# Kernel tuning notes

Hardware: AMD Instinct MI355X
Metric: run time of the kernel (lower is better)

Reference implementation:

```python
import jax, jax.numpy as jnp
import numpy as np

N_NODES = 50000
N_EDGES = 156000
D_IN = 512
D_OUT = 512
NUM_RELATIONS = 3
EPS = 0.0  # GIN eps, train_eps=False


def setup_inputs() -> dict:
    key = jax.random.key(0)
    ks = jax.random.split(key, 10)
    s = 1.0 / np.sqrt(D_IN)
    so = 1.0 / np.sqrt(D_OUT)
    return {
        "x": jax.random.normal(ks[0], (N_NODES, D_IN), dtype=jnp.float32),
        "edge_index": jax.random.randint(ks[1], (2, N_EDGES), 0, N_NODES, dtype=jnp.int64),
        "edge_type": jax.random.randint(ks[2], (N_EDGES,), 0, NUM_RELATIONS, dtype=jnp.int64),
        # self-loop linear
        "W_self": jax.random.uniform(ks[3], (D_IN, D_OUT), jnp.float32, -s, s),
        "b_self": jax.random.uniform(ks[4], (D_OUT,), jnp.float32, -s, s),
        # per-relation GIN MLP: Linear(D_IN,D_OUT) -> ReLU -> Linear(D_OUT,D_OUT)
        "W1": jax.random.uniform(ks[5], (NUM_RELATIONS, D_IN, D_OUT), jnp.float32, -s, s),
        "b1": jax.random.uniform(ks[6], (NUM_RELATIONS, D_OUT), jnp.float32, -s, s),
        "W2": jax.random.uniform(ks[7], (NUM_RELATIONS, D_OUT, D_OUT), jnp.float32, -so, so),
        "b2": jax.random.uniform(ks[8], (NUM_RELATIONS, D_OUT), jnp.float32, -so, so),
    }


def reference(x, edge_index, edge_type, W_self, b_self, W1, b1, W2, b2):
    n_nodes = x.shape[0]
    src, dst = edge_index[0], edge_index[1]
    x_src = x[src]  # [E, D_IN] single gather shared across relations
    out = x @ W_self + b_self  # self-loop linear, [N, D_OUT]
    for r in range(NUM_RELATIONS):
        mask = (edge_type == r).astype(x.dtype)[:, None]  # [E,1]
        # GIN sum-aggregation restricted to relation r edges
        agg = jax.ops.segment_sum(x_src * mask, dst, num_segments=n_nodes)  # [N, D_IN]
        h = (1.0 + EPS) * x + agg
        h = jnp.maximum(h @ W1[r] + b1[r], 0.0) @ W2[r] + b2[r]  # MLP
        out = out + h
    return out
```

## Files before the change

### kernel.cpp

```cpp
#include <hip/hip_runtime.h>
#include <hip/hip_bf16.h>

typedef __attribute__((ext_vector_type(8))) short bfrag_t;
typedef __attribute__((ext_vector_type(4))) float accum_t;
typedef __attribute__((ext_vector_type(8))) unsigned short us8_t;

static_assert(sizeof(bfrag_t) == 16, "frag size");

static constexpr int M_NODES = 50000;
static constexpr int E_EDGES = 156000;
static constexpr int MT256   = 196;
static constexpr int M_PAD   = MT256 * 256;

__device__ __forceinline__ unsigned short f2bf(float f) {
  unsigned int u = __float_as_uint(f);
  u = (u + 0x7FFFu + ((u >> 16) & 1u)) >> 16;
  return (unsigned short)u;
}
__device__ __forceinline__ float bf2f(unsigned short u) {
  return __uint_as_float(((unsigned int)u) << 16);
}

__device__ __forceinline__ void gll16(const unsigned short* g, unsigned short* l) {
  __builtin_amdgcn_global_load_lds(
      (const __attribute__((address_space(1))) void*)g,
      (__attribute__((address_space(3))) void*)l,
      16, 0, 0);
}

typedef __attribute__((ext_vector_type(2))) short s2v;
__device__ __forceinline__ void agg_atomic_add(unsigned int* p, unsigned int zv) {
#if __has_builtin(__builtin_amdgcn_global_atomic_fadd_v2bf16)
  s2v v;
  __builtin_memcpy(&v, &zv, 4);
  __builtin_amdgcn_global_atomic_fadd_v2bf16(
      (__attribute__((address_space(1))) s2v*)p, v);
#else
  unsigned int old = *p, assumed;
  do {
    assumed = old;
    float lo = bf2f((unsigned short)(assumed & 0xffffu)) +
               bf2f((unsigned short)(zv & 0xffffu));
    float hi = bf2f((unsigned short)(assumed >> 16)) +
               bf2f((unsigned short)(zv >> 16));
    unsigned int nv = (unsigned int)f2bf(lo) | ((unsigned int)f2bf(hi) << 16);
    old = atomicCAS(p, assumed, nv);
  } while (old != assumed);
#endif
}

__global__ void cast_w_kernel(const float* __restrict__ Wself,
                              const float* __restrict__ W1,
                              const float* __restrict__ W2,
                              const float* __restrict__ b2,
                              unsigned short* __restrict__ Wt1k,
                              unsigned short* __restrict__ Wt2k,
                              float* __restrict__ bias2) {
  int idx = blockIdx.x * 256 + threadIdx.x;
  if (idx < 1048576) {
    int j   = idx & 7;
    int n   = (idx >> 3) & 2047;
    int kcg = idx >> 14;
    int k   = kcg * 8 + j;
    float v = (n < 512)
        ? Wself[k * 512 + n]
        : W1[(size_t)((n - 512) >> 9) * 262144 + k * 512 + ((n - 512) & 511)];
    Wt1k[idx] = f2bf(v);
  } else if (idx < 1835008) {
    int j2  = idx - 1048576;
    int j   = j2 & 7;
    int n   = (j2 >> 3) & 511;
    int kcg = j2 >> 12;
    int kk  = kcg * 8 + j;
    Wt2k[j2] = f2bf(W2[(size_t)(kk >> 9) * 262144 + (size_t)(kk & 511) * 512 + n]);
  } else if (idx < 1835520) {
    int c = idx - 1835008;
    bias2[c] = b2[c] + b2[512 + c] + b2[1024 + c];
  }
}

__global__ __launch_bounds__(256) void cast_xk_kernel(const float* __restrict__ x,
                                                      unsigned short* __restrict__ xk) {
  __shared__ unsigned short T[32][520];
  const int b   = blockIdx.x;
  const int tid = threadIdx.x;
  for (int j = 0; j < 16; ++j) {
    int idx = j * 256 + tid;
    int row = idx >> 7, c4 = idx & 127;
    int grow = b * 32 + row;
    float4 v = (grow < M_NODES) ? ((const float4*)(x + (size_t)grow * 512))[c4]
                                : make_float4(0.f, 0.f, 0.f, 0.f);
    unsigned short* t = &T[row][c4 * 4];
    t[0] = f2bf(v.x); t[1] = f2bf(v.y); t[2] = f2bf(v.z); t[3] = f2bf(v.w);
  }
  __syncthreads();
  for (int j = 0; j < 8; ++j) {
    int idx = j * 256 + tid;
    int kc = idx >> 5, row = idx & 31;
    *(us8_t*)&xk[((size_t)kc * M_PAD + b * 32 + row) * 8] = *(const us8_t*)&T[row][kc * 8];
  }
}

__global__ void scatter_all_kernel(const unsigned short* __restrict__ Z,
                                   const int* __restrict__ ei,
                                   const int* __restrict__ et,
                                   unsigned short* __restrict__ agg) {
  int e    = blockIdx.x * 4 + (threadIdx.x >> 6);
  int lane = threadIdx.x & 63;
  if (e >= E_EDGES) return;
  int rel = et[e];
  int src = ei[e];
  int dst = ei[E_EDGES + e];
  const unsigned int* zs = (const unsigned int*)(Z + (size_t)src * 1536 + rel * 512);
  unsigned int* ad = (unsigned int*)(agg + (size_t)dst * 1536 + rel * 512);
  unsigned int v[4];
#pragma unroll
  for (int j = 0; j < 4; ++j) v[j] = zs[j * 64 + lane];
#pragma unroll
  for (int j = 0; j < 4; ++j) agg_atomic_add(ad + j * 64 + lane, v[j]);
}

__global__ void relu_all_kernel(unsigned short* __restrict__ Z,
                                const unsigned short* __restrict__ agg,
                                const float* __restrict__ b1) {
  int i = blockIdx.x * 256 + threadIdx.x;
  if (i >= M_NODES * 192) return;
  int c = (i % 192) * 8;
  us8_t z = ((const us8_t*)Z)[i];
  us8_t a = ((const us8_t*)agg)[i];
  us8_t o;
#pragma unroll
  for (int j = 0; j < 8; ++j) {
    float v = bf2f((unsigned short)z[j]) + bf2f((unsigned short)a[j]) + b1[c + j];
    o[j] = f2bf(fmaxf(v, 0.f));
  }
  ((us8_t*)Z)[i] = o;
}

__global__ __launch_bounds__(512, 4) void gemm1_kernel(
    const unsigned short* __restrict__ Ak,
    const unsigned short* __restrict__ Bk,
    float* __restrict__ outF,
    unsigned short* __restrict__ outB,
    const float* __restrict__ biasF) {
  constexpr int NT = 16, NTC = 16;
  __shared__ alignas(16) unsigned short L[3][12288];
  const int tid  = threadIdx.x;
  const int lane = tid & 63;
  const int wid  = tid >> 6;
  const int wr   = wid >> 1;
  const int wn   = wid & 1;
  const int fr   = lane & 15;
  const int kcl  = lane >> 4;

  constexpr int nwg = MT256 * NTC;
  constexpr int q   = nwg / 8;
  const int orig = blockIdx.x;
  const int swz  = (orig & 7) * q + (orig >> 3);
  const int tileM = (swz / NTC) * 256;
  const int tileN = (swz % NTC) * 128;

  accum_t acc[4][4] = {};

  const unsigned short* gA = Ak + ((size_t)(tid >> 8) * M_PAD + tileM + (tid & 255)) * 8;
  const unsigned short* gB = Bk + ((size_t)(tid >> 7) * 2048 + tileN + (tid & 127)) * 8;
  constexpr size_t AKT = (size_t)4 * M_PAD * 8;
  constexpr size_t A2  = (size_t)2 * M_PAD * 8;
  constexpr size_t BKT = (size_t)4 * 2048 * 8;

#define STG(buf, kt) do {                                            \
    gll16(gA + (size_t)(kt) * AKT,      &L[buf][tid * 8]);           \
    gll16(gA + (size_t)(kt) * AKT + A2, &L[buf][tid * 8 + 4096]);    \
    gll16(gB + (size_t)(kt) * BKT,      &L[buf][8192 + tid * 8]);    \
  } while (0)

  const int aoff = kcl * 2048 + (wr * 64 + fr) * 8;
  const int boff = 8192 + kcl * 1024 + (wn * 64 + fr) * 8;

  STG(0, 0); STG(1, 1);

  for (int kt = 0; kt < NT; ++kt) {
    if (kt + 1 < NT) asm volatile("s_waitcnt vmcnt(3)" ::: "memory");
    else             asm volatile("s_waitcnt vmcnt(0)" ::: "memory");
    __builtin_amdgcn_s_barrier();

    const unsigned short* Ls = &L[kt % 3][0];
    bfrag_t b[4], a[4];
#pragma unroll
    for (int nf = 0; nf < 4; ++nf)
      b[nf] = *(const bfrag_t*)(Ls + boff + nf * 128);
#pragma unroll
    for (int mf = 0; mf < 4; ++mf)
      a[mf] = *(const bfrag_t*)(Ls + aoff + mf * 128);
    if (kt + 2 < NT) STG((kt + 2) % 3, kt + 2);
    __builtin_amdgcn_s_setprio(1);
#pragma unroll
    for (int mf = 0; mf < 4; ++mf)
#pragma unroll
      for (int nf = 0; nf < 4; ++nf)
        acc[mf][nf] = __builtin_amdgcn_mfma_f32_16x16x32_bf16(a[mf], b[nf], acc[mf][nf], 0, 0, 0);
    __builtin_amdgcn_s_setprio(0);
  }
#undef STG

  __syncthreads();

  const int rq = lane >> 4;
  if (tileN >= 512) {
    unsigned short* Wld = &L[0][0] + wid * 4608;
#pragma unroll
    for (int mf = 0; mf < 4; ++mf)
#pragma unroll
      for (int nf = 0; nf < 4; ++nf)
#pragma unroll
        for (int p = 0; p < 4; ++p)
          Wld[(mf * 16 + rq * 4 + p) * 72 + nf * 16 + fr] = f2bf(acc[mf][nf][p]);
    const int r8 = lane >> 3;
    const int ch = lane & 7;
    const size_t zc = (size_t)(tileN - 512) + wn * 64 + ch * 8;
#pragma unroll
    for (int pass = 0; pass < 8; ++pass) {
      const int lrow = pass * 8 + r8;
      const int grow = tileM + wr * 64 + lrow;
      us8_t v = *(const us8_t*)&Wld[lrow * 72 + ch * 8];
      if (grow < M_NODES)
        *(us8_t*)&outB[(size_t)grow * 1536 + zc] = v;
    }
  } else {
#pragma unroll
    for (int nf = 0; nf < 4; ++nf) {
      const int col = tileN + wn * 64 + nf * 16 + fr;
      const float bv = biasF[col];
#pragma unroll
      for (int mf = 0; mf < 4; ++mf) {
        const int rbase = tileM + wr * 64 + mf * 16 + rq * 4;
#pragma unroll
        for (int p = 0; p < 4; ++p) {
          const int row = rbase + p;
          if (row < M_NODES)
            outF[(size_t)row * 512 + col] = acc[mf][nf][p] + bv;
        }
      }
    }
  }
}

__global__ __launch_bounds__(512, 4) void gemm2_kernel(
    const unsigned short* __restrict__ A,
    const unsigned short* __restrict__ Bk,
    float* __restrict__ outF,
    const float* __restrict__ bias) {
  constexpr int KTOT = 1536, NT = 48, NTC = 4;
  __shared__ alignas(16) unsigned short L[3][12288];
  const int tid  = threadIdx.x;
  const int lane = tid & 63;
  const int wid  = tid >> 6;
  const int wr   = wid >> 1;
  const int wn   = wid & 1;
  const int fr   = lane & 15;
  const int kcl  = lane >> 4;

  constexpr int nwg = MT256 * NTC;
  constexpr int q   = nwg / 8;
  const int orig = blockIdx.x;
  const int swz  = (orig & 7) * q + (orig >> 3);
  const int tileM = (swz / NTC) * 256;
  const int tileN = (swz % NTC) * 128;

  accum_t acc[4][4] = {};

  const int rowS = tid & 255;
  int arow = tileM + rowS; arow = arow < M_NODES ? arow : M_NODES - 1;
  const unsigned short* gA = A + (size_t)arow * KTOT + (tid >> 8) * 8;
  const unsigned short* gB = Bk + ((size_t)(tid >> 7) * 512 + tileN + (tid & 127)) * 8;
  constexpr size_t BKT = (size_t)4 * 512 * 8;

#define STG(buf, kt) do {                                          \
    gll16(gA + (kt) * 32,               &L[buf][tid * 8]);         \
    gll16(gA + (kt) * 32 + 16,          &L[buf][tid * 8 + 4096]);  \
    gll16(gB + (size_t)(kt) * BKT,      &L[buf][8192 + tid * 8]);  \
  } while (0)

  const int aoff = kcl * 2048 + (wr * 64 + fr) * 8;
  const int boff = 8192 + kcl * 1024 + (wn * 64 + fr) * 8;

  STG(0, 0); STG(1, 1);

  for (int kt = 0; kt < NT; ++kt) {
    if (kt + 1 < NT) asm volatile("s_waitcnt vmcnt(3)" ::: "memory");
    else             asm volatile("s_waitcnt vmcnt(0)" ::: "memory");
    __builtin_amdgcn_s_barrier();

    const unsigned short* Ls = &L[kt % 3][0];
    bfrag_t b[4], a[4];
#pragma unroll
    for (int nf = 0; nf < 4; ++nf)
      b[nf] = *(const bfrag_t*)(Ls + boff + nf * 128);
#pragma unroll
    for (int mf = 0; mf < 4; ++mf)
      a[mf] = *(const bfrag_t*)(Ls + aoff + mf * 128);
    if (kt + 2 < NT) STG((kt + 2) % 3, kt + 2);
    __builtin_amdgcn_s_setprio(1);
#pragma unroll
    for (int mf = 0; mf < 4; ++mf)
#pragma unroll
      for (int nf = 0; nf < 4; ++nf)
        acc[mf][nf] = __builtin_amdgcn_mfma_f32_16x16x32_bf16(a[mf], b[nf], acc[mf][nf], 0, 0, 0);
    __builtin_amdgcn_s_setprio(0);
  }
#undef STG

  const int rq = lane >> 4;
#pragma unroll
  for (int nf = 0; nf < 4; ++nf) {
    const int col = tileN + wn * 64 + nf * 16 + fr;
    const float bv = bias[col];
#pragma unroll
    for (int mf = 0; mf < 4; ++mf) {
      const int rbase = tileM + wr * 64 + mf * 16 + rq * 4;
#pragma unroll
      for (int p = 0; p < 4; ++p) {
        const int row = rbase + p;
        if (row < M_NODES)
          outF[(size_t)row * 512 + col] += acc[mf][nf][p] + bv;
      }
    }
  }
}

extern "C" void kernel_launch(void* const* d_in, const int* in_sizes, int n_in,
                              void* d_out, int out_size, void* d_ws, size_t ws_size,
                              hipStream_t stream) {
  const float* x     = (const float*)d_in[0];
  const int*   ei    = (const int*)d_in[1];
  const int*   et    = (const int*)d_in[2];
  const float* Wself = (const float*)d_in[3];
  const float* bself = (const float*)d_in[4];
  const float* W1    = (const float*)d_in[5];
  const float* b1    = (const float*)d_in[6];
  const float* W2    = (const float*)d_in[7];
  const float* b2    = (const float*)d_in[8];
  float* out = (float*)d_out;

  char* ws = (char*)d_ws;
  unsigned short* xk    = (unsigned short*)ws;
  unsigned short* agg   = (unsigned short*)ws;
  unsigned short* Z     = (unsigned short*)(ws + 153600000);
  unsigned short* Wt1k  = (unsigned short*)(ws + 307200000);
  unsigned short* Wt2k  = (unsigned short*)(ws + 309297152);
  float*          bias2 = (float*)(ws + 310870016);

  cast_w_kernel<<<7171, 256, 0, stream>>>(Wself, W1, W2, b2, Wt1k, Wt2k, bias2);
  cast_xk_kernel<<<M_PAD / 32, 256, 0, stream>>>(x, xk);

  gemm1_kernel<<<MT256 * 16, 512, 0, stream>>>(xk, Wt1k, out, Z, bself);

  hipMemsetAsync(agg, 0, (size_t)M_NODES * 1536 * sizeof(unsigned short), stream);
  scatter_all_kernel<<<E_EDGES / 4, 256, 0, stream>>>(Z, ei, et, agg);
  relu_all_kernel<<<(M_NODES * 192 + 255) / 256, 256, 0, stream>>>(Z, agg, b1);

  gemm2_kernel<<<MT256 * 4, 512, 0, stream>>>(Z, Wt2k, out, bias2);
}
```

Measured before the change: 671.9 us.

## Transpose relu output into k-chunked layout and seed agg by copying Z

The relu kernel now reads only the aggregate buffer and writes its output through shared memory in a k-chunked, M-padded layout, so gemm2 can stage A with the same contiguous loads it uses for B. The aggregate buffer is initialised with a device copy of Z instead of a memset, which folds the self term into agg and lets relu skip reading Z. gemm1 gains an extra output pointer, but it is passed Z twice, so it writes the same data to the same address. The copy moves more bytes than a memset did, and Zk aliases Z, so relu overwrites Z after scatter has finished reading it.

Result: faster. 599.2 us (-10.8%).

```diff
diff --git a/kernel.cpp b/kernel.cpp
--- a/kernel.cpp
+++ b/kernel.cpp
@@ -120,21 +120,38 @@
   for (int j = 0; j < 4; ++j) agg_atomic_add(ad + j * 64 + lane, v[j]);
 }
 
-__global__ void relu_all_kernel(unsigned short* __restrict__ Z,
-                                const unsigned short* __restrict__ agg,
-                                const float* __restrict__ b1) {
-  int i = blockIdx.x * 256 + threadIdx.x;
-  if (i >= M_NODES * 192) return;
-  int c = (i % 192) * 8;
-  us8_t z = ((const us8_t*)Z)[i];
-  us8_t a = ((const us8_t*)agg)[i];
-  us8_t o;
-#pragma unroll
-  for (int j = 0; j < 8; ++j) {
-    float v = bf2f((unsigned short)z[j]) + bf2f((unsigned short)a[j]) + b1[c + j];
-    o[j] = f2bf(fmaxf(v, 0.f));
-  }
-  ((us8_t*)Z)[i] = o;
+__global__ __launch_bounds__(256) void relu_t_kernel(
+    const unsigned short* __restrict__ agg,
+    const float* __restrict__ b1,
+    unsigned short* __restrict__ Zk) {
+  __shared__ unsigned short T[16][1544];
+  const int b   = blockIdx.x;
+  const int tid = threadIdx.x;
+#pragma unroll
+  for (int j = 0; j < 12; ++j) {
+    int idx = j * 256 + tid;
+    int row = idx / 192, cc = idx % 192;
+    int grow = b * 16 + row;
+    us8_t o;
+    if (grow < M_NODES) {
+      us8_t a = ((const us8_t*)agg)[(size_t)grow * 192 + cc];
+      const float* bb = b1 + cc * 8;
+#pragma unroll
+      for (int q = 0; q < 8; ++q)
+        o[q] = f2bf(fmaxf(bf2f((unsigned short)a[q]) + bb[q], 0.f));
+    } else {
+#pragma unroll
+      for (int q = 0; q < 8; ++q) o[q] = 0;
+    }
+    *(us8_t*)&T[row][cc * 8] = o;
+  }
+  __syncthreads();
+#pragma unroll
+  for (int j = 0; j < 12; ++j) {
+    int idx = j * 256 + tid;
+    int kc = idx >> 4, row = idx & 15;
+    *(us8_t*)&Zk[((size_t)kc * M_PAD + b * 16 + row) * 8] = *(const us8_t*)&T[row][kc * 8];
+  }
 }
 
 __global__ __launch_bounds__(512, 4) void gemm1_kernel(
@@ -142,6 +159,7 @@
     const unsigned short* __restrict__ Bk,
     float* __restrict__ outF,
     unsigned short* __restrict__ outB,
+    unsigned short* __restrict__ aggB,
     const float* __restrict__ biasF) {
   constexpr int NT = 16, NTC = 16;
   __shared__ alignas(16) unsigned short L[3][12288];
@@ -223,8 +241,10 @@
       const int lrow = pass * 8 + r8;
       const int grow = tileM + wr * 64 + lrow;
       us8_t v = *(const us8_t*)&Wld[lrow * 72 + ch * 8];
-      if (grow < M_NODES)
+      if (grow < M_NODES) {
         *(us8_t*)&outB[(size_t)grow * 1536 + zc] = v;
+        *(us8_t*)&aggB[(size_t)grow * 1536 + zc] = v;
+      }
     }
   } else {
 #pragma unroll
@@ -246,11 +266,11 @@
 }
 
 __global__ __launch_bounds__(512, 4) void gemm2_kernel(
-    const unsigned short* __restrict__ A,
+    const unsigned short* __restrict__ Ak,
     const unsigned short* __restrict__ Bk,
     float* __restrict__ outF,
     const float* __restrict__ bias) {
-  constexpr int KTOT = 1536, NT = 48, NTC = 4;
+  constexpr int NT = 48, NTC = 4;
   __shared__ alignas(16) unsigned short L[3][12288];
   const int tid  = threadIdx.x;
   const int lane = tid & 63;
@@ -269,16 +289,16 @@
 
   accum_t acc[4][4] = {};
 
-  const int rowS = tid & 255;
-  int arow = tileM + rowS; arow = arow < M_NODES ? arow : M_NODES - 1;
-  const unsigned short* gA = A + (size_t)arow * KTOT + (tid >> 8) * 8;
+  const unsigned short* gA = Ak + ((size_t)(tid >> 8) * M_PAD + tileM + (tid & 255)) * 8;
   const unsigned short* gB = Bk + ((size_t)(tid >> 7) * 512 + tileN + (tid & 127)) * 8;
+  constexpr size_t AKT = (size_t)4 * M_PAD * 8;
+  constexpr size_t A2  = (size_t)2 * M_PAD * 8;
   constexpr size_t BKT = (size_t)4 * 512 * 8;
 
-#define STG(buf, kt) do {                                          \
-    gll16(gA + (kt) * 32,               &L[buf][tid * 8]);         \
-    gll16(gA + (kt) * 32 + 16,          &L[buf][tid * 8 + 4096]);  \
-    gll16(gB + (size_t)(kt) * BKT,      &L[buf][8192 + tid * 8]);  \
+#define STG(buf, kt) do {                                            \
+    gll16(gA + (size_t)(kt) * AKT,      &L[buf][tid * 8]);           \
+    gll16(gA + (size_t)(kt) * AKT + A2, &L[buf][tid * 8 + 4096]);    \
+    gll16(gB + (size_t)(kt) * BKT,      &L[buf][8192 + tid * 8]);    \
   } while (0)
 
   const int aoff = kcl * 2048 + (wr * 64 + fr) * 8;
@@ -346,6 +366,7 @@
   unsigned short* xk    = (unsigned short*)ws;
   unsigned short* agg   = (unsigned short*)ws;
   unsigned short* Z     = (unsigned short*)(ws + 153600000);
+  unsigned short* Zk    = (unsigned short*)(ws + 153600000);
   unsigned short* Wt1k  = (unsigned short*)(ws + 307200000);
   unsigned short* Wt2k  = (unsigned short*)(ws + 309297152);
   float*          bias2 = (float*)(ws + 310870016);
@@ -353,11 +374,13 @@
   cast_w_kernel<<<7171, 256, 0, stream>>>(Wself, W1, W2, b2, Wt1k, Wt2k, bias2);
   cast_xk_kernel<<<M_PAD / 32, 256, 0, stream>>>(x, xk);
 
-  gemm1_kernel<<<MT256 * 16, 512, 0, stream>>>(xk, Wt1k, out, Z, bself);
-
-  hipMemsetAsync(agg, 0, (size_t)M_NODES * 1536 * sizeof(unsigned short), stream);
+  gemm1_kernel<<<MT256 * 16, 512, 0, stream>>>(xk, Wt1k, out, Z, Z , bself);
+
+  hipMemcpyAsync(agg, Z, (size_t)M_NODES * 1536 * sizeof(unsigned short),
+                 hipMemcpyDeviceToDevice, stream);
+
   scatter_all_kernel<<<E_EDGES / 4, 256, 0, stream>>>(Z, ei, et, agg);
-  relu_all_kernel<<<(M_NODES * 192 + 255) / 256, 256, 0, stream>>>(Z, agg, b1);
-
-  gemm2_kernel<<<MT256 * 4, 512, 0, stream>>>(Z, Wt2k, out, bias2);
-}
+  relu_t_kernel<<<M_PAD / 16, 256, 0, stream>>>(agg, b1, Zk);
+
+  gemm2_kernel<<<MT256 * 4, 512, 0, stream>>>(Zk, Wt2k, out, bias2);
+}
```
